# Optimization experiments

Hardware: AMD Instinct MI355X
Metric: run time of the kernel (lower is better)

## Reference

```python
import jax, jax.numpy as jnp
import numpy as np


def setup_inputs() -> dict:
    key = jax.random.key(0)
    k1, k2 = jax.random.split(key)
    B, D, N = 8, 3, 4096
    srcs = jax.random.normal(k1, (B, D, N), dtype=jnp.float32)
    tgts = jax.random.normal(k2, (B, D, N), dtype=jnp.float32)
    return {"srcs": srcs, "tgts": tgts}


def _chamfer(srcs, tgts):
    # srcs, tgts: [B, D, N] -> points [B, N, D]
    s = jnp.swapaxes(srcs, 1, 2)  # [B, Ns, D]
    t = jnp.swapaxes(tgts, 1, 2)  # [B, Nt, D]
    # squared norms (equals diag of self-distance bmm in original)
    rs = jnp.sum(s * s, axis=-1)  # [B, Ns]
    rt = jnp.sum(t * t, axis=-1)  # [B, Nt]
    st = jnp.einsum("bnd,bmd->bnm", s, t)  # [B, Ns, Nt]
    # P[b,i,j] = |s_i|^2 + |t_j|^2 - 2 s_i . t_j
    P = rs[:, :, None] + rt[:, None, :] - 2.0 * st
    # min over src dim (axis 1) mean + min over tgt dim (axis 2) mean
    return jnp.min(P, axis=1).mean() + jnp.min(P, axis=2).mean()


def reference(srcs, tgts):
    return _chamfer(srcs, tgts)
```

## Files before the change

kernel.cpp:

```cpp
#include <hip/hip_runtime.h>


#define CD_B 8
#define CD_N 4096
#define BLK 256
#define TCH 32
#define TPB (CD_N / TCH)
#define QQ 8
#define QPB (BLK * QQ)
#define QCH (CD_N / QPB)
#define NQ (2 * CD_B * CD_N)

__global__ __launch_bounds__(BLK) void cd_partial(
    const float* __restrict__ srcs, const float* __restrict__ tgts,
    float* __restrict__ ws, float* __restrict__ out) {
  const int bid = blockIdx.x;
  const int tc  = bid & (TCH - 1);
  const int qc  = (bid >> 5) & (QCH - 1);
  const int b   = (bid >> 6) & (CD_B - 1);
  const int dir = bid >> 9;

  const float* qb = (dir ? tgts : srcs) + b * 3 * CD_N;
  const float* tb = (dir ? srcs : tgts) + b * 3 * CD_N;

  __shared__ float4 T[TPB];
  const int tid = threadIdx.x;
  if (tid < TPB) {
    int gj = tc * TPB + tid;
    float x = tb[gj], y = tb[CD_N + gj], z = tb[2 * CD_N + gj];
    T[tid] = make_float4(x, y, z, x * x + y * y + z * z);
  }
  if (bid == 0 && tid == 0) out[0] = 0.0f;
  __syncthreads();

  float sx[QQ], sy[QQ], sz[QQ];
  const int q0 = qc * QPB + tid;
#pragma unroll
  for (int qq = 0; qq < QQ; ++qq) {
    int q = q0 + qq * BLK;
    sx[qq] = qb[q];
    sy[qq] = qb[CD_N + q];
    sz[qq] = qb[2 * CD_N + q];
  }

  float mm[QQ];
#pragma unroll
  for (int qq = 0; qq < QQ; ++qq) mm[qq] = 3.4e38f;

  for (int j = 0; j < TPB; j += 2) {
    float4 p0 = T[j];
    float4 p1 = T[j + 1];
#pragma unroll
    for (int qq = 0; qq < QQ; ++qq) {
      float st0 = fmaf(sx[qq], p0.x, fmaf(sy[qq], p0.y, sz[qq] * p0.z));
      float st1 = fmaf(sx[qq], p1.x, fmaf(sy[qq], p1.y, sz[qq] * p1.z));
      float v0 = fmaf(-2.0f, st0, p0.w);
      float v1 = fmaf(-2.0f, st1, p1.w);
      mm[qq] = fminf(mm[qq], fminf(v0, v1));
    }
  }

  const int gqbase = (dir * CD_B + b) * CD_N + qc * QPB + tid;
  float* wrow = ws + (size_t)tc * NQ;
#pragma unroll
  for (int qq = 0; qq < QQ; ++qq) {
    float ssq = fmaf(sx[qq], sx[qq], fmaf(sy[qq], sy[qq], sz[qq] * sz[qq]));
    wrow[gqbase + qq * BLK] = mm[qq] + ssq;
  }
}

__global__ __launch_bounds__(BLK) void cd_reduce(
    const float* __restrict__ ws, float* __restrict__ out) {
  const int q = blockIdx.x * BLK + threadIdx.x;
  float m0 = ws[q];
  float m1 = ws[(size_t)1 * NQ + q];
#pragma unroll
  for (int tc = 2; tc < TCH; tc += 2) {
    m0 = fminf(m0, ws[(size_t)tc * NQ + q]);
    m1 = fminf(m1, ws[(size_t)(tc + 1) * NQ + q]);
  }
  float m = fminf(m0, m1);

  for (int off = 32; off; off >>= 1) m += __shfl_down(m, off, 64);
  __shared__ float wsum[BLK / 64];
  if ((threadIdx.x & 63) == 0) wsum[threadIdx.x >> 6] = m;
  __syncthreads();
  if (threadIdx.x == 0) {
    float s = (wsum[0] + wsum[1]) + (wsum[2] + wsum[3]);
    atomicAdd(out, s * (1.0f / (float)(CD_B * CD_N)));
  }
}

extern "C" void kernel_launch(void* const* d_in, const int* in_sizes, int n_in,
                              void* d_out, int out_size, void* d_ws, size_t ws_size,
                              hipStream_t stream) {
  const float* srcs = (const float*)d_in[0];
  const float* tgts = (const float*)d_in[1];
  float* out = (float*)d_out;
  float* ws = (float*)d_ws;

  cd_partial<<<2 * CD_B * QCH * TCH, BLK, 0, stream>>>(srcs, tgts, ws, out);
  cd_reduce<<<NQ / BLK, BLK, 0, stream>>>(ws, out);
}
```

Before: 86.48 us.

## Precompute packed -2x candidate table and use packed FMA with min3

```diff
diff --git a/kernel.cpp b/kernel.cpp
--- a/kernel.cpp
+++ b/kernel.cpp
@@ -10,53 +10,86 @@
 #define QPB (BLK * QQ)
 #define QCH (CD_N / QPB)
 #define NQ (2 * CD_B * CD_N)
+#define NG (CD_N / 2)
+#define MINS_FLOATS (TCH * NQ)
+
+typedef __attribute__((ext_vector_type(2))) float f32x2;
+
+__device__ __forceinline__ f32x2 pk_fma_sv(f32x2 a_v, f32x2 b_s, f32x2 c_v) {
+  f32x2 d;
+  asm("v_pk_fma_f32 %0, %1, %2, %3" : "=v"(d) : "v"(a_v), "s"(b_s), "v"(c_v));
+  return d;
+}
+
+__device__ __forceinline__ float min3f(float m, float a, float b) {
+  asm("v_min3_f32 %0, %1, %2, %0" : "+v"(m) : "v"(a), "v"(b));
+  return m;
+}
+
+__global__ __launch_bounds__(BLK) void cd_prep(
+    const float* __restrict__ srcs, const float* __restrict__ tgts,
+    float4* __restrict__ P) {
+  const int g   = blockIdx.x * BLK + threadIdx.x;
+  const int grp = g & (NG - 1);
+  const int b   = (g >> 11) & (CD_B - 1);
+  const int dir = g >> 14;
+  const float* tb = (dir ? srcs : tgts) + b * 3 * CD_N;
+  const int j = grp * 2;
+  float x0 = tb[j],            x1 = tb[j + 1];
+  float y0 = tb[CD_N + j],     y1 = tb[CD_N + j + 1];
+  float z0 = tb[2 * CD_N + j], z1 = tb[2 * CD_N + j + 1];
+  float w0 = fmaf(x0, x0, fmaf(y0, y0, z0 * z0));
+  float w1 = fmaf(x1, x1, fmaf(y1, y1, z1 * z1));
+  float4* Pp = P + ((size_t)(dir * CD_B + b) * NG + grp) * 2;
+  Pp[0] = make_float4(-2.f * x0, -2.f * x1, -2.f * y0, -2.f * y1);
+  Pp[1] = make_float4(-2.f * z0, -2.f * z1, w0, w1);
+}
 
 __global__ __launch_bounds__(BLK) void cd_partial(
     const float* __restrict__ srcs, const float* __restrict__ tgts,
-    float* __restrict__ ws, float* __restrict__ out) {
+    const float4* __restrict__ P, float* __restrict__ ws,
+    float* __restrict__ out) {
   const int bid = blockIdx.x;
   const int tc  = bid & (TCH - 1);
   const int qc  = (bid >> 5) & (QCH - 1);
   const int b   = (bid >> 6) & (CD_B - 1);
   const int dir = bid >> 9;
+  const int tid = threadIdx.x;
 
   const float* qb = (dir ? tgts : srcs) + b * 3 * CD_N;
-  const float* tb = (dir ? srcs : tgts) + b * 3 * CD_N;
+  if (bid == 0 && tid == 0) out[0] = 0.0f;
 
-  __shared__ float4 T[TPB];
-  const int tid = threadIdx.x;
-  if (tid < TPB) {
-    int gj = tc * TPB + tid;
-    float x = tb[gj], y = tb[CD_N + gj], z = tb[2 * CD_N + gj];
-    T[tid] = make_float4(x, y, z, x * x + y * y + z * z);
-  }
-  if (bid == 0 && tid == 0) out[0] = 0.0f;
-  __syncthreads();
-
-  float sx[QQ], sy[QQ], sz[QQ];
+  f32x2 qx2[QQ], qy2[QQ], qz2[QQ];
   const int q0 = qc * QPB + tid;
 #pragma unroll
   for (int qq = 0; qq < QQ; ++qq) {
     int q = q0 + qq * BLK;
-    sx[qq] = qb[q];
-    sy[qq] = qb[CD_N + q];
-    sz[qq] = qb[2 * CD_N + q];
+    float sx = qb[q], sy = qb[CD_N + q], sz = qb[2 * CD_N + q];
+    qx2[qq] = (f32x2){sx, sx};
+    qy2[qq] = (f32x2){sy, sy};
+    qz2[qq] = (f32x2){sz, sz};
   }
 
   float mm[QQ];
 #pragma unroll
   for (int qq = 0; qq < QQ; ++qq) mm[qq] = 3.4e38f;
 
-  for (int j = 0; j < TPB; j += 2) {
-    float4 p0 = T[j];
-    float4 p1 = T[j + 1];
+  const float4* __restrict__ Pp =
+      P + ((size_t)(dir * CD_B + b) * NG + tc * (TPB / 2)) * 2;
+#pragma unroll 2
+  for (int g = 0; g < TPB / 2; ++g) {
+    float4 ab = Pp[2 * g];
+    float4 cd = Pp[2 * g + 1];
+    f32x2 cx2 = (f32x2){ab.x, ab.y};
+    f32x2 cy2 = (f32x2){ab.z, ab.w};
+    f32x2 cz2 = (f32x2){cd.x, cd.y};
+    f32x2 cwv = (f32x2){cd.z, cd.w};
 #pragma unroll
     for (int qq = 0; qq < QQ; ++qq) {
-      float st0 = fmaf(sx[qq], p0.x, fmaf(sy[qq], p0.y, sz[qq] * p0.z));
-      float st1 = fmaf(sx[qq], p1.x, fmaf(sy[qq], p1.y, sz[qq] * p1.z));
-      float v0 = fmaf(-2.0f, st0, p0.w);
-      float v1 = fmaf(-2.0f, st1, p1.w);
-      mm[qq] = fminf(mm[qq], fminf(v0, v1));
+      f32x2 acc = pk_fma_sv(qz2[qq], cz2, cwv);
+      acc = pk_fma_sv(qy2[qq], cy2, acc);
+      acc = pk_fma_sv(qx2[qq], cx2, acc);
+      mm[qq] = min3f(mm[qq], acc.x, acc.y);
     }
   }
 
@@ -64,7 +97,8 @@
   float* wrow = ws + (size_t)tc * NQ;
 #pragma unroll
   for (int qq = 0; qq < QQ; ++qq) {
-    float ssq = fmaf(sx[qq], sx[qq], fmaf(sy[qq], sy[qq], sz[qq] * sz[qq]));
+    float sx = qx2[qq].x, sy = qy2[qq].x, sz = qz2[qq].x;
+    float ssq = fmaf(sx, sx, fmaf(sy, sy, sz * sz));
     wrow[gqbase + qq * BLK] = mm[qq] + ssq;
   }
 }
@@ -97,8 +131,10 @@
   const float* srcs = (const float*)d_in[0];
   const float* tgts = (const float*)d_in[1];
   float* out = (float*)d_out;
-  float* ws = (float*)d_ws;
+  float* ws_mins = (float*)d_ws;
+  float4* P = (float4*)((char*)d_ws + (size_t)MINS_FLOATS * 4);
 
-  cd_partial<<<2 * CD_B * QCH * TCH, BLK, 0, stream>>>(srcs, tgts, ws, out);
-  cd_reduce<<<NQ / BLK, BLK, 0, stream>>>(ws, out);
+  cd_prep<<<(2 * CD_B * NG) / BLK, BLK, 0, stream>>>(srcs, tgts, P);
+  cd_partial<<<2 * CD_B * QCH * TCH, BLK, 0, stream>>>(srcs, tgts, P, ws_mins, out);
+  cd_reduce<<<NQ / BLK, BLK, 0, stream>>>(ws_mins, out);
 }
```

New measurement: 85.91 us. About the same (-0.7%).

## Precompute scaled target float4s, read them uniformly from global, use v_min3

Applied to the files above, without the earlier changes.

```diff
diff --git a/kernel.cpp b/kernel.cpp
--- a/kernel.cpp
+++ b/kernel.cpp
@@ -6,32 +6,43 @@
 #define BLK 256
 #define TCH 32
 #define TPB (CD_N / TCH)
-#define QQ 8
+#define QQ 4
 #define QPB (BLK * QQ)
 #define QCH (CD_N / QPB)
 #define NQ (2 * CD_B * CD_N)
+#define MINS_FLOATS (TCH * NQ)
 
-__global__ __launch_bounds__(BLK) void cd_partial(
+__device__ __forceinline__ float min3f(float m, float a, float b) {
+  asm("v_min3_f32 %0, %1, %2, %0" : "+v"(m) : "v"(a), "v"(b));
+  return m;
+}
+
+__global__ __launch_bounds__(BLK) void cd_prep(
     const float* __restrict__ srcs, const float* __restrict__ tgts,
-    float* __restrict__ ws, float* __restrict__ out) {
+    float4* __restrict__ P, float* __restrict__ out) {
+  const int g   = blockIdx.x * BLK + threadIdx.x;
+  const int j   = g & (CD_N - 1);
+  const int b   = (g >> 12) & (CD_B - 1);
+  const int dir = g >> 15;
+  const float* tb = (dir ? srcs : tgts) + b * 3 * CD_N;
+  float x = tb[j], y = tb[CD_N + j], z = tb[2 * CD_N + j];
+  float w = fmaf(x, x, fmaf(y, y, z * z));
+  P[(size_t)(dir * CD_B + b) * CD_N + j] =
+      make_float4(-2.f * x, -2.f * y, -2.f * z, w);
+  if (g == 0) out[0] = 0.0f;
+}
+
+__global__ __launch_bounds__(BLK, 8) void cd_partial(
+    const float* __restrict__ srcs, const float* __restrict__ tgts,
+    const float4* __restrict__ P, float* __restrict__ ws) {
   const int bid = blockIdx.x;
   const int tc  = bid & (TCH - 1);
   const int qc  = (bid >> 5) & (QCH - 1);
-  const int b   = (bid >> 6) & (CD_B - 1);
-  const int dir = bid >> 9;
+  const int b   = (bid >> 7) & (CD_B - 1);
+  const int dir = bid >> 10;
+  const int tid = threadIdx.x;
 
   const float* qb = (dir ? tgts : srcs) + b * 3 * CD_N;
-  const float* tb = (dir ? srcs : tgts) + b * 3 * CD_N;
-
-  __shared__ float4 T[TPB];
-  const int tid = threadIdx.x;
-  if (tid < TPB) {
-    int gj = tc * TPB + tid;
-    float x = tb[gj], y = tb[CD_N + gj], z = tb[2 * CD_N + gj];
-    T[tid] = make_float4(x, y, z, x * x + y * y + z * z);
-  }
-  if (bid == 0 && tid == 0) out[0] = 0.0f;
-  __syncthreads();
 
   float sx[QQ], sy[QQ], sz[QQ];
   const int q0 = qc * QPB + tid;
@@ -47,16 +58,17 @@
 #pragma unroll
   for (int qq = 0; qq < QQ; ++qq) mm[qq] = 3.4e38f;
 
-  for (int j = 0; j < TPB; j += 2) {
-    float4 p0 = T[j];
-    float4 p1 = T[j + 1];
+  const float4* __restrict__ Pp =
+      P + (size_t)(dir * CD_B + b) * CD_N + tc * TPB;
+#pragma unroll 4
+  for (int g = 0; g < TPB / 2; ++g) {
+    float4 t0 = Pp[2 * g];
+    float4 t1 = Pp[2 * g + 1];
 #pragma unroll
     for (int qq = 0; qq < QQ; ++qq) {
-      float st0 = fmaf(sx[qq], p0.x, fmaf(sy[qq], p0.y, sz[qq] * p0.z));
-      float st1 = fmaf(sx[qq], p1.x, fmaf(sy[qq], p1.y, sz[qq] * p1.z));
-      float v0 = fmaf(-2.0f, st0, p0.w);
-      float v1 = fmaf(-2.0f, st1, p1.w);
-      mm[qq] = fminf(mm[qq], fminf(v0, v1));
+      float v0 = fmaf(sx[qq], t0.x, fmaf(sy[qq], t0.y, fmaf(sz[qq], t0.z, t0.w)));
+      float v1 = fmaf(sx[qq], t1.x, fmaf(sy[qq], t1.y, fmaf(sz[qq], t1.z, t1.w)));
+      mm[qq] = min3f(mm[qq], v0, v1);
     }
   }
 
@@ -97,8 +109,10 @@
   const float* srcs = (const float*)d_in[0];
   const float* tgts = (const float*)d_in[1];
   float* out = (float*)d_out;
-  float* ws = (float*)d_ws;
+  float* ws_mins = (float*)d_ws;
+  float4* P = (float4*)((char*)d_ws + (size_t)MINS_FLOATS * 4);
 
-  cd_partial<<<2 * CD_B * QCH * TCH, BLK, 0, stream>>>(srcs, tgts, ws, out);
-  cd_reduce<<<NQ / BLK, BLK, 0, stream>>>(ws, out);
+  cd_prep<<<NQ / BLK, BLK, 0, stream>>>(srcs, tgts, P, out);
+  cd_partial<<<2 * CD_B * QCH * TCH, BLK, 0, stream>>>(srcs, tgts, P, ws_mins);
+  cd_reduce<<<NQ / BLK, BLK, 0, stream>>>(ws_mins, out);
 }
```

Measured after the change: 92.36 us. +6.8%, slower.
